# Performance work log

Hardware: AMD Instinct MI355X
Metric: run time of the kernel (lower is better)

The kernel has to match this reference:

```python
import jax, jax.numpy as jnp
import numpy as np

N_NODES = 100000
N_EDGES = 1600000
IN_C, HID, OUT_C = 128, 128, 64
BN_EPS = 1e-5


def gcn_conv(x, W, b, src, dst):
    # PyG GCNConv(normalize=False): linear first, then sum-aggregate over edges
    m = x @ W                                   # [N, out_dim]
    agg = jax.ops.segment_sum(m[src], dst, num_segments=N_NODES)  # scatter-add by dst
    return agg + b


def batch_norm(h, gamma, beta):
    mu = jnp.mean(h, axis=0)
    var = jnp.var(h, axis=0)
    return (h - mu) * jax.lax.rsqrt(var + BN_EPS) * gamma + beta


def setup_inputs() -> dict:
    key = jax.random.key(0)
    ks = jax.random.split(key, 8)
    x = jax.random.normal(ks[0], (N_NODES, IN_C), dtype=jnp.float32)
    edge_src = jax.random.randint(ks[1], (N_EDGES,), 0, N_NODES, dtype=jnp.int32)
    edge_dst = jnp.sort(jax.random.randint(ks[2], (N_EDGES,), 0, N_NODES, dtype=jnp.int32))
    def glorot(k, shape):
        lim = float(np.sqrt(6.0 / (shape[0] + shape[1])))
        return jax.random.uniform(k, shape, jnp.float32, -lim, lim)
    return {
        "x": x, "edge_src": edge_src, "edge_dst": edge_dst,
        "W0": glorot(ks[3], (IN_C, HID)), "b0": jnp.zeros((HID,), jnp.float32),
        "W1": glorot(ks[4], (HID, HID)), "b1": jnp.zeros((HID,), jnp.float32),
        "W2": glorot(ks[5], (HID, OUT_C)), "b2": jnp.zeros((OUT_C,), jnp.float32),
        "g0": jnp.ones((HID,), jnp.float32), "be0": jnp.zeros((HID,), jnp.float32),
        "g1": jnp.ones((HID,), jnp.float32), "be1": jnp.zeros((HID,), jnp.float32),
    }


def reference(x, edge_src, edge_dst, W0, b0, W1, b1, W2, b2, g0, be0, g1, be1):
    # layer 0: conv -> BN -> residual (dims match: 128==128) -> ReLU (dropout p=0)
    h = gcn_conv(x, W0, b0, edge_src, edge_dst)
    h = batch_norm(h, g0, be0)
    h = h + x  # residual, in_channels == hidden_channels
    x1 = jax.nn.relu(h)
    # layer 1
    h = gcn_conv(x1, W1, b1, edge_src, edge_dst)
    h = batch_norm(h, g1, be1)
    h = h + x1
    x2 = jax.nn.relu(h)
    # final layer: conv only
    return gcn_conv(x2, W2, b2, edge_src, edge_dst)
```

## Files before the change

kernel.cpp:

```cpp
#include <hip/hip_runtime.h>

#define BN_EPS 1e-5f

typedef __attribute__((ext_vector_type(8))) short bf16x8;
typedef __attribute__((ext_vector_type(4))) float f32x4;

__device__ __forceinline__ short f2bf(float f) {
    union { float f; unsigned u; } v; v.f = f;
    unsigned r = (v.u + 0x7fffu + ((v.u >> 16) & 1u)) >> 16;
    return (short)r;
}
__device__ __forceinline__ float bflo(unsigned d) {
    union { unsigned u; float f; } v; v.u = d << 16; return v.f;
}
__device__ __forceinline__ float bfhi(unsigned d) {
    union { unsigned u; float f; } v; v.u = d & 0xffff0000u; return v.f;
}

__global__ __launch_bounds__(256) void build_off_k(const int* __restrict__ dst,
                                                   int* __restrict__ off, int E, int N) {
    int i = blockIdx.x * 256 + threadIdx.x;
    if (i > E) return;
    int cur  = (i < E) ? dst[i] : N;
    int prev = (i == 0) ? -1 : dst[i - 1];
    for (int n = prev + 1; n <= cur; ++n) off[n] = i;
}

__global__ void zero_k(float* p, int n) {
    int i = blockIdx.x * blockDim.x + threadIdx.x;
    if (i < n) p[i] = 0.f;
}

__global__ __launch_bounds__(256) void wtrans_k(const float* __restrict__ W,
                                                short* __restrict__ Wt, int K, int C) {
    int i = blockIdx.x * 256 + threadIdx.x;
    if (i >= K * C) return;
    int c = i / K, k = i % K;
    Wt[i] = f2bf(W[k * C + c]);
}

template <int OUTC>
__global__ __launch_bounds__(256) void mgemm_k(const float* __restrict__ X,
                                               const short* __restrict__ Wt,
                                               short* __restrict__ M, int N) {
    constexpr int NR = OUTC / 16;
    __shared__ short sW[OUTC][136];

    const int tid = threadIdx.x;
    for (int q = tid; q < OUTC * 16; q += 256) {
        int r = q >> 4, s = q & 15;
        *(int4*)&sW[r][s * 8] = ((const int4*)Wt)[q];
    }
    __syncthreads();

    const int wave = tid >> 6, lane = tid & 63;
    const int lr = lane & 15, lg = lane >> 4;
    const int row0 = blockIdx.x * 128 + wave * 32;

    f32x4 acc[2][NR];
    #pragma unroll
    for (int m = 0; m < 2; ++m)
        #pragma unroll
        for (int n = 0; n < NR; ++n) acc[m][n] = (f32x4){0.f, 0.f, 0.f, 0.f};

    #pragma unroll
    for (int kk = 0; kk < 4; ++kk) {
        bf16x8 a[2];
        #pragma unroll
        for (int m = 0; m < 2; ++m) {
            int row = row0 + m * 16 + lr;
            float4 x0 = make_float4(0.f, 0.f, 0.f, 0.f), x1 = x0;
            if (row < N) {
                const float4* p = (const float4*)&X[(size_t)row * 128 + kk * 32 + lg * 8];
                x0 = p[0]; x1 = p[1];
            }
            a[m][0] = f2bf(x0.x); a[m][1] = f2bf(x0.y);
            a[m][2] = f2bf(x0.z); a[m][3] = f2bf(x0.w);
            a[m][4] = f2bf(x1.x); a[m][5] = f2bf(x1.y);
            a[m][6] = f2bf(x1.z); a[m][7] = f2bf(x1.w);
        }
        #pragma unroll
        for (int n = 0; n < NR; ++n) {
            bf16x8 b = *(const bf16x8*)&sW[n * 16 + lr][kk * 32 + lg * 8];
            acc[0][n] = __builtin_amdgcn_mfma_f32_16x16x32_bf16(a[0], b, acc[0][n], 0, 0, 0);
            acc[1][n] = __builtin_amdgcn_mfma_f32_16x16x32_bf16(a[1], b, acc[1][n], 0, 0, 0);
        }
    }

    #pragma unroll
    for (int m = 0; m < 2; ++m)
        #pragma unroll
        for (int r = 0; r < 4; ++r) {
            int row = row0 + m * 16 + lg * 4 + r;
            if (row < N) {
                #pragma unroll
                for (int n = 0; n < NR; ++n)
                    M[(size_t)row * OUTC + n * 16 + lr] = f2bf(acc[m][n][r]);
            }
        }
}

template <int C>
__global__ __launch_bounds__(256) void agg_k(const short* __restrict__ M,
                                             const int* __restrict__ src,
                                             const int* __restrict__ off,
                                             const float* __restrict__ bias,
                                             float* __restrict__ H, int N) {
    const int lane = threadIdx.x & 63;
    const int node = blockIdx.x * 4 + (threadIdx.x >> 6);
    if (node >= N) return;
    const int e0 = off[node], e1 = off[node + 1];

    if constexpr (C == 128) {
        const unsigned* M32 = (const unsigned*)M;
        float2 acc = make_float2(0.f, 0.f);
        for (int base = e0; base < e1; base += 64) {
            int e = base + lane;
            int s = (e < e1) ? src[e] : 0;
            int cnt = min(64, e1 - base);
            int i = 0;
            for (; i + 4 <= cnt; i += 4) {
                int s0 = __shfl(s, i),     s1 = __shfl(s, i + 1);
                int s2 = __shfl(s, i + 2), s3 = __shfl(s, i + 3);
                unsigned d0 = M32[s0 * 64 + lane];
                unsigned d1 = M32[s1 * 64 + lane];
                unsigned d2 = M32[s2 * 64 + lane];
                unsigned d3 = M32[s3 * 64 + lane];
                acc.x += (bflo(d0) + bflo(d1)) + (bflo(d2) + bflo(d3));
                acc.y += (bfhi(d0) + bfhi(d1)) + (bfhi(d2) + bfhi(d3));
            }
            for (; i < cnt; ++i) {
                int si = __shfl(s, i);
                unsigned d = M32[si * 64 + lane];
                acc.x += bflo(d); acc.y += bfhi(d);
            }
        }
        float2 bv = *(const float2*)&bias[lane * 2];
        *(float2*)&H[node * 128 + lane * 2] = make_float2(acc.x + bv.x, acc.y + bv.y);
    } else {
        const unsigned short* M16 = (const unsigned short*)M;
        float acc = 0.f;
        for (int base = e0; base < e1; base += 64) {
            int e = base + lane;
            int s = (e < e1) ? src[e] : 0;
            int cnt = min(64, e1 - base);
            int i = 0;
            for (; i + 4 <= cnt; i += 4) {
                int s0 = __shfl(s, i),     s1 = __shfl(s, i + 1);
                int s2 = __shfl(s, i + 2), s3 = __shfl(s, i + 3);
                float v0 = bflo((unsigned)M16[s0 * 64 + lane] << 16 >> 16 | ((unsigned)M16[s0 * 64 + lane] << 16));
                v0 = bflo((unsigned)M16[s0 * 64 + lane]);
                float v1 = bflo((unsigned)M16[s1 * 64 + lane]);
                float v2 = bflo((unsigned)M16[s2 * 64 + lane]);
                float v3 = bflo((unsigned)M16[s3 * 64 + lane]);
                acc += (v0 + v1) + (v2 + v3);
            }
            for (; i < cnt; ++i) {
                int si = __shfl(s, i);
                acc += bflo((unsigned)M16[si * 64 + lane]);
            }
        }
        H[node * 64 + lane] = acc + bias[lane];
    }
}

__global__ __launch_bounds__(256) void stats_k(const float* __restrict__ H,
                                               float* __restrict__ stats, int N) {
    const int c = threadIdx.x & 127;
    const int half = threadIdx.x >> 7;
    float sum = 0.f, sq = 0.f;
    for (int r = blockIdx.x * 2 + half; r < N; r += gridDim.x * 2) {
        float v = H[r * 128 + c];
        sum += v; sq = fmaf(v, v, sq);
    }
    __shared__ float sS[128], sQ[128];
    if (half) { sS[c] = sum; sQ[c] = sq; }
    __syncthreads();
    if (!half) {
        atomicAdd(&stats[c], sum + sS[c]);
        atomicAdd(&stats[128 + c], sq + sQ[c]);
    }
}

__global__ void bnfin_k(const float* __restrict__ stats, const float* __restrict__ gamma,
                        const float* __restrict__ beta, float* __restrict__ ss, float invN) {
    int c = threadIdx.x;
    float mu  = stats[c] * invN;
    float var = fmaf(-mu, mu, stats[128 + c] * invN);
    float sc  = gamma[c] * rsqrtf(var + BN_EPS);
    ss[c]       = sc;
    ss[128 + c] = fmaf(-mu, sc, beta[c]);
}

__global__ __launch_bounds__(256) void apply_k(const float* H,
                                               const float* __restrict__ R,
                                               const float* __restrict__ ss,
                                               float* Xn, int n4) {
    int i = blockIdx.x * 256 + threadIdx.x;
    if (i >= n4) return;
    int c4 = (i & 31) << 2;
    float4 h = ((const float4*)H)[i];
    float4 r = ((const float4*)R)[i];
    float4 o;
    o.x = fmaxf(fmaf(h.x, ss[c4 + 0], ss[128 + c4 + 0]) + r.x, 0.f);
    o.y = fmaxf(fmaf(h.y, ss[c4 + 1], ss[128 + c4 + 1]) + r.y, 0.f);
    o.z = fmaxf(fmaf(h.z, ss[c4 + 2], ss[128 + c4 + 2]) + r.z, 0.f);
    o.w = fmaxf(fmaf(h.w, ss[c4 + 3], ss[128 + c4 + 3]) + r.w, 0.f);
    ((float4*)Xn)[i] = o;
}

extern "C" void kernel_launch(void* const* d_in, const int* in_sizes, int n_in,
                              void* d_out, int out_size, void* d_ws, size_t ws_size,
                              hipStream_t stream) {
    const float* x   = (const float*)d_in[0];
    const int*   src = (const int*)d_in[1];
    const int*   dst = (const int*)d_in[2];
    const float* W0  = (const float*)d_in[3];
    const float* b0  = (const float*)d_in[4];
    const float* W1  = (const float*)d_in[5];
    const float* b1  = (const float*)d_in[6];
    const float* W2  = (const float*)d_in[7];
    const float* b2  = (const float*)d_in[8];
    const float* g0  = (const float*)d_in[9];
    const float* be0 = (const float*)d_in[10];
    const float* g1  = (const float*)d_in[11];
    const float* be1 = (const float*)d_in[12];
    float* out = (float*)d_out;

    const int N = in_sizes[0] / 128;
    const int E = in_sizes[1];

    char*  ws   = (char*)d_ws;
    size_t bufB = (size_t)N * 128 * sizeof(float);
    short* Mb = (short*)(ws);
    float* B  = (float*)(ws + bufB);
    float* Cb = (float*)(ws + 2 * bufB);
    size_t p  = 3 * bufB;
    int*   off = (int*)(ws + p);
    p += ((size_t)(N + 1) * sizeof(int) + 255) & ~(size_t)255;
    float* stats0 = (float*)(ws + p); p += 1024;
    float* stats1 = (float*)(ws + p); p += 1024;
    float* ss     = (float*)(ws + p); p += 1024;
    short* Wt0    = (short*)(ws + p); p += 128 * 128 * 2;
    short* Wt1    = (short*)(ws + p); p += 128 * 128 * 2;
    short* Wt2    = (short*)(ws + p); p += 128 * 64 * 2;

    const dim3 blk(256);
    const int gGemm  = (N + 127) / 128;
    const int gAgg   = (N + 3) / 4;
    const int gApply = (N * 32 + 255) / 256;
    const float invN = 1.f / (float)N;

    zero_k<<<2, blk, 0, stream>>>(stats0, 512);
    wtrans_k<<<64, blk, 0, stream>>>(W0, Wt0, 128, 128);
    wtrans_k<<<64, blk, 0, stream>>>(W1, Wt1, 128, 128);
    wtrans_k<<<32, blk, 0, stream>>>(W2, Wt2, 128, 64);
    build_off_k<<<(E + 256) / 256, blk, 0, stream>>>(dst, off, E, N);

    mgemm_k<128><<<gGemm, blk, 0, stream>>>(x, Wt0, Mb, N);
    agg_k<128><<<gAgg, blk, 0, stream>>>(Mb, src, off, b0, B, N);
    stats_k<<<1024, blk, 0, stream>>>(B, stats0, N);
    bnfin_k<<<1, 128, 0, stream>>>(stats0, g0, be0, ss, invN);
    apply_k<<<gApply, blk, 0, stream>>>(B, x, ss, B, N * 32);

    mgemm_k<128><<<gGemm, blk, 0, stream>>>(B, Wt1, Mb, N);
    agg_k<128><<<gAgg, blk, 0, stream>>>(Mb, src, off, b1, Cb, N);
    stats_k<<<1024, blk, 0, stream>>>(Cb, stats1, N);
    bnfin_k<<<1, 128, 0, stream>>>(stats1, g1, be1, ss, invN);
    apply_k<<<gApply, blk, 0, stream>>>(Cb, B, ss, Cb, N * 32);

    mgemm_k<64><<<gGemm, blk, 0, stream>>>(Cb, Wt2, Mb, N);
    agg_k<64><<<gAgg, blk, 0, stream>>>(Mb, src, off, b2, out, N);
}
```

Measured before the change: 373.0 us.

## Store GEMM output in 16-column planes and aggregate per plane for cache locality

```diff
diff --git a/kernel.cpp b/kernel.cpp
--- a/kernel.cpp
+++ b/kernel.cpp
@@ -42,7 +42,7 @@
 template <int OUTC>
 __global__ __launch_bounds__(256) void mgemm_k(const float* __restrict__ X,
                                                const short* __restrict__ Wt,
-                                               short* __restrict__ M, int N) {
+                                               short* __restrict__ Mp, int N) {
     constexpr int NR = OUTC / 16;
     __shared__ short sW[OUTC][136];
 
@@ -56,6 +56,7 @@
     const int wave = tid >> 6, lane = tid & 63;
     const int lr = lane & 15, lg = lane >> 4;
     const int row0 = blockIdx.x * 128 + wave * 32;
+    const size_t planeStride = (size_t)N * 16;
 
     f32x4 acc[2][NR];
     #pragma unroll
@@ -95,72 +96,57 @@
             if (row < N) {
                 #pragma unroll
                 for (int n = 0; n < NR; ++n)
-                    M[(size_t)row * OUTC + n * 16 + lr] = f2bf(acc[m][n][r]);
+                    Mp[(size_t)n * planeStride + row * 16 + lr] = f2bf(acc[m][n][r]);
             }
         }
 }
 
 template <int C>
-__global__ __launch_bounds__(256) void agg_k(const short* __restrict__ M,
-                                             const int* __restrict__ src,
-                                             const int* __restrict__ off,
-                                             const float* __restrict__ bias,
-                                             float* __restrict__ H, int N) {
-    const int lane = threadIdx.x & 63;
-    const int node = blockIdx.x * 4 + (threadIdx.x >> 6);
-    if (node >= N) return;
-    const int e0 = off[node], e1 = off[node + 1];
-
-    if constexpr (C == 128) {
-        const unsigned* M32 = (const unsigned*)M;
+__global__ __launch_bounds__(256) void pagg_k(const short* __restrict__ Mp,
+                                              const int* __restrict__ src,
+                                              const int* __restrict__ off,
+                                              const float* __restrict__ bias,
+                                              float* __restrict__ H, int N) {
+    constexpr int NP = C / 16;
+    const int plane = blockIdx.x % NP;
+    const int nb    = blockIdx.x / NP;
+    const unsigned* __restrict__ P =
+        (const unsigned*)Mp + (size_t)plane * N * 8;
+
+    const int wave = threadIdx.x >> 6, lane = threadIdx.x & 63;
+    const int e8 = lane >> 3, c = lane & 7;
+
+    #pragma unroll
+    for (int w = 0; w < 2; ++w) {
+        const int node = nb * 8 + wave * 2 + w;
+        if (node >= N) continue;
+        const int e0 = off[node], e1 = off[node + 1];
+
         float2 acc = make_float2(0.f, 0.f);
         for (int base = e0; base < e1; base += 64) {
             int e = base + lane;
             int s = (e < e1) ? src[e] : 0;
             int cnt = min(64, e1 - base);
-            int i = 0;
-            for (; i + 4 <= cnt; i += 4) {
-                int s0 = __shfl(s, i),     s1 = __shfl(s, i + 1);
-                int s2 = __shfl(s, i + 2), s3 = __shfl(s, i + 3);
-                unsigned d0 = M32[s0 * 64 + lane];
-                unsigned d1 = M32[s1 * 64 + lane];
-                unsigned d2 = M32[s2 * 64 + lane];
-                unsigned d3 = M32[s3 * 64 + lane];
-                acc.x += (bflo(d0) + bflo(d1)) + (bflo(d2) + bflo(d3));
-                acc.y += (bfhi(d0) + bfhi(d1)) + (bfhi(d2) + bfhi(d3));
+            int ngrp = (cnt + 7) >> 3;
+            #pragma unroll 4
+            for (int j = 0; j < ngrp; ++j) {
+                int idx = (j << 3) + e8;
+                int si = __shfl(s, idx);
+                unsigned d = (idx < cnt) ? P[(size_t)si * 8 + c] : 0u;
+                acc.x += bflo(d);
+                acc.y += bfhi(d);
             }
-            for (; i < cnt; ++i) {
-                int si = __shfl(s, i);
-                unsigned d = M32[si * 64 + lane];
-                acc.x += bflo(d); acc.y += bfhi(d);
-            }
-        }
-        float2 bv = *(const float2*)&bias[lane * 2];
-        *(float2*)&H[node * 128 + lane * 2] = make_float2(acc.x + bv.x, acc.y + bv.y);
-    } else {
-        const unsigned short* M16 = (const unsigned short*)M;
-        float acc = 0.f;
-        for (int base = e0; base < e1; base += 64) {
-            int e = base + lane;
-            int s = (e < e1) ? src[e] : 0;
-            int cnt = min(64, e1 - base);
-            int i = 0;
-            for (; i + 4 <= cnt; i += 4) {
-                int s0 = __shfl(s, i),     s1 = __shfl(s, i + 1);
-                int s2 = __shfl(s, i + 2), s3 = __shfl(s, i + 3);
-                float v0 = bflo((unsigned)M16[s0 * 64 + lane] << 16 >> 16 | ((unsigned)M16[s0 * 64 + lane] << 16));
-                v0 = bflo((unsigned)M16[s0 * 64 + lane]);
-                float v1 = bflo((unsigned)M16[s1 * 64 + lane]);
-                float v2 = bflo((unsigned)M16[s2 * 64 + lane]);
-                float v3 = bflo((unsigned)M16[s3 * 64 + lane]);
-                acc += (v0 + v1) + (v2 + v3);
-            }
-            for (; i < cnt; ++i) {
-                int si = __shfl(s, i);
-                acc += bflo((unsigned)M16[si * 64 + lane]);
-            }
-        }
-        H[node * 64 + lane] = acc + bias[lane];
+        }
+        #pragma unroll
+        for (int dlt = 8; dlt < 64; dlt <<= 1) {
+            acc.x += __shfl_xor(acc.x, dlt);
+            acc.y += __shfl_xor(acc.y, dlt);
+        }
+        if (e8 == 0) {
+            float2 bv = *(const float2*)&bias[plane * 16 + c * 2];
+            *(float2*)&H[(size_t)node * C + plane * 16 + c * 2] =
+                make_float2(acc.x + bv.x, acc.y + bv.y);
+        }
     }
 }
 
@@ -246,9 +232,10 @@
     short* Wt2    = (short*)(ws + p); p += 128 * 64 * 2;
 
     const dim3 blk(256);
-    const int gGemm  = (N + 127) / 128;
-    const int gAgg   = (N + 3) / 4;
-    const int gApply = (N * 32 + 255) / 256;
+    const int gGemm   = (N + 127) / 128;
+    const int gAgg128 = 8 * ((N + 7) / 8);
+    const int gAgg64  = 4 * ((N + 7) / 8);
+    const int gApply  = (N * 32 + 255) / 256;
     const float invN = 1.f / (float)N;
 
     zero_k<<<2, blk, 0, stream>>>(stats0, 512);
@@ -258,17 +245,17 @@
     build_off_k<<<(E + 256) / 256, blk, 0, stream>>>(dst, off, E, N);
 
     mgemm_k<128><<<gGemm, blk, 0, stream>>>(x, Wt0, Mb, N);
-    agg_k<128><<<gAgg, blk, 0, stream>>>(Mb, src, off, b0, B, N);
+    pagg_k<128><<<gAgg128, blk, 0, stream>>>(Mb, src, off, b0, B, N);
     stats_k<<<1024, blk, 0, stream>>>(B, stats0, N);
     bnfin_k<<<1, 128, 0, stream>>>(stats0, g0, be0, ss, invN);
     apply_k<<<gApply, blk, 0, stream>>>(B, x, ss, B, N * 32);
 
     mgemm_k<128><<<gGemm, blk, 0, stream>>>(B, Wt1, Mb, N);
-    agg_k<128><<<gAgg, blk, 0, stream>>>(Mb, src, off, b1, Cb, N);
+    pagg_k<128><<<gAgg128, blk, 0, stream>>>(Mb, src, off, b1, Cb, N);
     stats_k<<<1024, blk, 0, stream>>>(Cb, stats1, N);
     bnfin_k<<<1, 128, 0, stream>>>(stats1, g1, be1, ss, invN);
     apply_k<<<gApply, blk, 0, stream>>>(Cb, B, ss, Cb, N * 32);
 
     mgemm_k<64><<<gGemm, blk, 0, stream>>>(Cb, Wt2, Mb, N);
-    agg_k<64><<<gAgg, blk, 0, stream>>>(Mb, src, off, b2, out, N);
-}
+    pagg_k<64><<<gAgg64, blk, 0, stream>>>(Mb, src, off, b2, out, N);
+}
```

After: 689.2 us. +84.8%, slower.
